# Optimization experiments

Measured on AMD Instinct MI355X. Metric: run time of the kernel, lower is better.

Reference implementation:

```python
import jax, jax.numpy as jnp
import numpy as np


def _hippo_dplr(n):
    # HiPPO-LegS -> NPLR -> DPLR (diagonal plus low rank) init, as in S4
    pr = np.sqrt(1.0 + 2.0 * np.arange(n))
    A = -(np.tril(pr[:, None] * pr[None, :]) - np.diag(np.arange(n)))
    p = np.sqrt(np.arange(n) + 0.5)
    b = np.sqrt(2.0 * np.arange(n) + 1.0)
    S = A + p[:, None] * p[None, :]
    lam_re = np.full(n, np.mean(np.diagonal(S)))
    lam_im, V = np.linalg.eigh(S * -1j)  # S*-1j is Hermitian
    p_c = V.conj().T @ p.astype(np.complex128)
    b_c = V.conj().T @ b.astype(np.complex128)
    return lam_re, lam_im, p_c, b_c


def setup_inputs():
    B, L, H, N = 4, 1024, 512, 64
    key = jax.random.key(0)
    kx, kc, ks, k1, k2 = jax.random.split(key, 5)
    lam_re, lam_im, p_c, b_c = _hippo_dplr(N)
    c = jax.random.normal(kc, (N, 2)) * (0.5 ** 0.5)
    f32 = lambda a: jnp.asarray(a, dtype=jnp.float32)
    return {
        'x': jax.random.normal(kx, (B, L, H), dtype=jnp.float32),
        'norm_weight': jnp.ones((H,), jnp.float32),
        'norm_bias': jnp.zeros((H,), jnp.float32),
        'lambda_re': f32(lam_re), 'lambda_im': f32(lam_im),
        'p_re': f32(p_c.real), 'p_im': f32(p_c.imag),
        'b_re': f32(b_c.real), 'b_im': f32(b_c.imag),
        'c_re': c[:, 0].astype(jnp.float32), 'c_im': c[:, 1].astype(jnp.float32),
        'd': jnp.ones((), jnp.float32),
        'log_step': jax.random.uniform(ks, (), jnp.float32, float(np.log(0.001)), float(np.log(0.1))),
        'out_w': (jax.random.normal(k1, (H, H), jnp.float32) / np.sqrt(H)).astype(jnp.float32),
        'out_b': jnp.zeros((H,), jnp.float32),
        'out2_w': (jax.random.normal(k2, (H, H), jnp.float32) / np.sqrt(H)).astype(jnp.float32),
        'out2_b': jnp.zeros((H,), jnp.float32),
    }


def reference(x, norm_weight, norm_bias, lambda_re, lambda_im, p_re, p_im,
              b_re, b_im, c_re, c_im, d, log_step, out_w, out_b, out2_w, out2_b):
    Bsz, L, H = x.shape
    skip = x
    # LayerNorm over channel dim (eps=1e-5, eqx default)
    mu = jnp.mean(x, -1, keepdims=True)
    var = jnp.mean((x - mu) ** 2, -1, keepdims=True)
    xn = (x - mu) / jnp.sqrt(var + 1e-5) * norm_weight + norm_bias
    # --- S4 DPLR bilinear discretization ---
    lam = (lambda_re + 1j * lambda_im).astype(jnp.complex64)
    p = (p_re + 1j * p_im).astype(jnp.complex64)
    b = (b_re + 1j * b_im).astype(jnp.complex64)
    c = (c_re + 1j * c_im).astype(jnp.complex64)
    step = jnp.exp(log_step).astype(jnp.complex64)
    N = lam.shape[0]
    I = jnp.eye(N, dtype=jnp.complex64)
    A = jnp.diag(lam) - p[:, None] * p[None, :].conj()
    A0 = (2.0 / step) * I + A
    Dinv = jnp.diag(1.0 / ((2.0 / step) - lam))
    qcD = p.conj()[None, :] @ Dinv           # [1,N]
    Dp = Dinv @ p[:, None]                   # [N,1]
    A1 = Dinv - (Dp @ qcD) / (1.0 + (qcD @ p[:, None]))  # Woodbury
    Ab = A1 @ A0                             # [N,N] discrete state matrix
    Bb = 2.0 * (A1 @ b[:, None])[:, 0]       # [N]
    # --- sequential state-space scan over time, vectorized over (B,H) lanes ---
    u = xn.astype(jnp.complex64)             # [B,L,H]

    def step_fn(state, u_t):                 # state: [B,H,N], u_t: [B,H]
        new = jnp.einsum('nm,bhm->bhn', Ab, state) + u_t[..., None] * Bb
        return new, jnp.einsum('n,bhn->bh', c, new).real

    init = jnp.zeros((Bsz, H, N), jnp.complex64)
    _, ys = jax.lax.scan(step_fn, init, jnp.moveaxis(u, 1, 0))  # ys: [L,B,H]
    y = jnp.moveaxis(ys, 0, 1) + d * xn      # feedthrough term
    # --- GELU + GLU-style gated output projection, residual ---
    y = jax.nn.gelu(y)
    gate = jax.nn.sigmoid(y @ out2_w.T + out2_b)
    return skip + (y @ out_w.T + out_b) * gate
```

## Files before the change

kernel.cpp:

```cpp
#include <hip/hip_runtime.h>
#include <hip/hip_bf16.h>
#include <math.h>

#define HDIM 512
#define LSEQ 1024
#define BSZ  4

typedef __attribute__((ext_vector_type(8))) short short8;
typedef __attribute__((ext_vector_type(4))) float floatx4;
typedef _Float16 half8 __attribute__((ext_vector_type(8)));

__device__ __forceinline__ float2 cmul(float2 a, float2 b) {
  float2 r;
  r.x = a.x * b.x - a.y * b.y;
  r.y = a.x * b.y + a.y * b.x;
  return r;
}
__device__ __forceinline__ float2 cadd(float2 a, float2 b) {
  float2 r; r.x = a.x + b.x; r.y = a.y + b.y; return r;
}
__device__ __forceinline__ float2 cfma(float2 a, float2 b, float2 c) {
  c.x += a.x * b.x - a.y * b.y;
  c.y += a.x * b.y + a.y * b.x;
  return c;
}
__device__ __forceinline__ ushort f2h(float f) {
  _Float16 h = (_Float16)f;
  return *(ushort*)&h;
}

__global__ __launch_bounds__(576) void stage1_kernel(
    const float* __restrict__ x, const float* __restrict__ nw,
    const float* __restrict__ nb, float* __restrict__ xn,
    const float* __restrict__ lre, const float* __restrict__ lim,
    const float* __restrict__ pre, const float* __restrict__ pim,
    const float* __restrict__ bre, const float* __restrict__ bim,
    const float* __restrict__ cre, const float* __restrict__ cim,
    const float* __restrict__ logstep, float* __restrict__ Kout,
    const float* __restrict__ w1, const float* __restrict__ w2,
    ushort* __restrict__ Wst) {
  __shared__ float2 Ldab[64], Lu[64], Lr[64], LBb[64];
  __shared__ float2 Rv[2048];
  __shared__ float2 Wv[2048];
  int tid = threadIdx.x;
  int wv = tid >> 6;
  int lane = tid & 63;

  if (blockIdx.x != 0) {
    int row = (blockIdx.x - 1) * 9 + wv;
    if (row < BSZ * LSEQ) {
      const float* xr = x + (size_t)row * HDIM;
      float4 v0 = ((const float4*)xr)[lane];
      float4 v1 = ((const float4*)xr)[lane + 64];
      float s  = v0.x + v0.y + v0.z + v0.w + v1.x + v1.y + v1.z + v1.w;
      float ss = v0.x*v0.x + v0.y*v0.y + v0.z*v0.z + v0.w*v0.w
               + v1.x*v1.x + v1.y*v1.y + v1.z*v1.z + v1.w*v1.w;
      #pragma unroll
      for (int m = 1; m < 64; m <<= 1) { s += __shfl_xor(s, m); ss += __shfl_xor(ss, m); }
      float mu   = s * (1.0f / HDIM);
      float var  = ss * (1.0f / HDIM) - mu * mu;
      float rstd = rsqrtf(var + 1e-5f);
      float4 w0 = ((const float4*)nw)[lane];
      float4 w1v = ((const float4*)nw)[lane + 64];
      float4 b0 = ((const float4*)nb)[lane];
      float4 b1 = ((const float4*)nb)[lane + 64];
      float4 o0, o1;
      o0.x = (v0.x - mu) * rstd * w0.x + b0.x;
      o0.y = (v0.y - mu) * rstd * w0.y + b0.y;
      o0.z = (v0.z - mu) * rstd * w0.z + b0.z;
      o0.w = (v0.w - mu) * rstd * w0.w + b0.w;
      o1.x = (v1.x - mu) * rstd * w1v.x + b1.x;
      o1.y = (v1.y - mu) * rstd * w1v.y + b1.y;
      o1.z = (v1.z - mu) * rstd * w1v.z + b1.z;
      o1.w = (v1.w - mu) * rstd * w1v.w + b1.w;
      float* xo = xn + (size_t)row * HDIM;
      ((float4*)xo)[lane] = o0;
      ((float4*)xo)[lane + 64] = o1;
    }
    int idx = (blockIdx.x - 1) * 576 + tid;
    if (idx < 65536) {
      int e0 = idx * 8;
      int n = e0 >> 9, k0 = e0 & 511;
      const float* Wr = (n < 512) ? (w1 + (size_t)n * 512 + k0)
                                  : (w2 + (size_t)(n - 512) * 512 + k0);
      ushort tmp[8];
      #pragma unroll
      for (int q = 0; q < 8; q++) tmp[q] = f2h(Wr[q]);
      *(short8*)&Wst[e0] = *(short8*)tmp;
    }
    return;
  }

  if (tid < 64) {
    int n = tid;
    float step = expf(logstep[0]);
    float g = 2.0f / step;
    float lr = lre[n], li = lim[n];
    float pr = pre[n], pi = pim[n];
    float br = bre[n], bi = bim[n];
    float den  = (g - lr) * (g - lr) + li * li;
    float dinr = (g - lr) / den, dini = li / den;
    float dabr = (g + lr) * dinr - li * dini;
    float dabi = (g + lr) * dini + li * dinr;
    float ur = dinr * pr - dini * pi;
    float ui = dinr * pi + dini * pr;
    float qr = pr * dinr + pi * dini;
    float qi = pr * dini - pi * dinr;
    float pm2 = pr * pr + pi * pi;
    float betr = pm2 * dinr, beti = pm2 * dini;
    float gar = qr * br - qi * bi;
    float gai = qr * bi + qi * br;
    #pragma unroll
    for (int m = 1; m < 64; m <<= 1) {
      betr += __shfl_xor(betr, m); beti += __shfl_xor(beti, m);
      gar  += __shfl_xor(gar, m);  gai  += __shfl_xor(gai, m);
    }
    float obr = 1.0f + betr, obi = beti;
    float ob2 = obr * obr + obi * obi;
    float kr = -2.0f * g * obr / ob2;
    float ki =  2.0f * g * obi / ob2;
    float rr = kr * qr - ki * qi;
    float ri = kr * qi + ki * qr;
    float tgr = (gar * obr + gai * obi) / ob2;
    float tgi = (gai * obr - gar * obi) / ob2;
    float dbr = dinr * br - dini * bi;
    float dbi = dinr * bi + dini * br;
    float Bbr = 2.0f * (dbr - (ur * tgr - ui * tgi));
    float Bbi = 2.0f * (dbi - (ur * tgi + ui * tgr));
    float2 t;
    t.x = dabr; t.y = dabi; Ldab[n] = t;
    t.x = ur;   t.y = ui;   Lu[n]   = t;
    t.x = rr;   t.y = ri;   Lr[n]   = t;
    t.x = Bbr;  t.y = Bbi;  LBb[n]  = t;
  }
  if (wv == 8) { float2 cc; cc.x = cre[lane]; cc.y = cim[lane]; Rv[lane] = cc; }
  __syncthreads();

  int g8 = lane >> 3;
  int q8 = lane & 7;
  int jm = wv * 8 + g8;
  float2 cv[8];

  if (wv < 8) {
    float2 dab[8], u[8], rn[8];
    #pragma unroll
    for (int ii = 0; ii < 8; ii++) {
      int n = q8 * 8 + ii;
      dab[ii] = Ldab[n]; u[ii] = Lu[n]; rn[ii] = Lr[n];
    }
    float2 rj = Lr[jm];
    #pragma unroll
    for (int ii = 0; ii < 8; ii++) {
      int n = q8 * 8 + ii;
      cv[ii] = cmul(u[ii], rj);
      if (n == jm) cv[ii] = cadd(cv[ii], dab[ii]);
    }
    for (int s = 0; s < 31; s++) {
      float2 part; part.x = 0.f; part.y = 0.f;
      #pragma unroll
      for (int ii = 0; ii < 8; ii++) part = cfma(rn[ii], cv[ii], part);
      #pragma unroll
      for (int m = 1; m < 8; m <<= 1) {
        part.x += __shfl_xor(part.x, m);
        part.y += __shfl_xor(part.y, m);
      }
      #pragma unroll
      for (int ii = 0; ii < 8; ii++) {
        float2 nc = cmul(dab[ii], cv[ii]);
        cv[ii] = cfma(u[ii], part, nc);
      }
    }
  } else {
    float2 dab0 = Ldab[lane], u0 = Lu[lane], r0 = Lr[lane];
    float2 w = LBb[lane];
    Wv[lane * 32 + 0] = w;
    for (int b = 1; b < 32; b++) {
      float dr = r0.x * w.x - r0.y * w.y;
      float di = r0.x * w.y + r0.y * w.x;
      #pragma unroll
      for (int m = 1; m < 64; m <<= 1) { dr += __shfl_xor(dr, m); di += __shfl_xor(di, m); }
      float2 nw2;
      nw2.x = dab0.x * w.x - dab0.y * w.y + u0.x * dr - u0.y * di;
      nw2.y = dab0.x * w.y + dab0.y * w.x + u0.x * di + u0.y * dr;
      w = nw2;
      Wv[lane * 32 + b] = w;
    }
  }
  __syncthreads();

  for (int a = 1; a < 32; a++) {
    if (wv < 8) {
      float2 part; part.x = 0.f; part.y = 0.f;
      #pragma unroll
      for (int ii = 0; ii < 8; ii++) {
        float2 Rk = Rv[(a - 1) * 64 + q8 * 8 + ii];
        part = cfma(Rk, cv[ii], part);
      }
      #pragma unroll
      for (int m = 1; m < 8; m <<= 1) {
        part.x += __shfl_xor(part.x, m);
        part.y += __shfl_xor(part.y, m);
      }
      if (q8 == 0) Rv[a * 64 + jm] = part;
    }
    __syncthreads();
  }

  for (int midx = tid; midx < 1024; midx += 576) {
    int a = midx >> 5, b = midx & 31;
    float acc = 0.f;
    for (int n = 0; n < 64; n++) {
      float2 R = Rv[a * 64 + n];
      float2 W = Wv[n * 32 + b];
      acc += R.x * W.x - R.y * W.y;
    }
    Kout[midx] = acc;
  }
}

__global__ __launch_bounds__(256) void prep_kernel(
    const float* __restrict__ xn, const float* __restrict__ K,
    ushort* __restrict__ Uhi, ushort* __restrict__ Thi) {
  __shared__ float tile[64][65];
  int blk = blockIdx.x;
  int tid = threadIdx.x;
  if (blk < 512) {
    int ht = blk & 7, lt = (blk >> 3) & 15, b = blk >> 7;
    #pragma unroll
    for (int q = 0; q < 16; q++) {
      int idx = q * 256 + tid;
      int r = idx >> 6, c = idx & 63;
      tile[r][c] = xn[((size_t)(b * LSEQ + lt * 64 + r)) * HDIM + ht * 64 + c];
    }
    __syncthreads();
    #pragma unroll
    for (int q = 0; q < 16; q++) {
      int idx = q * 256 + tid;
      int r = idx >> 6, c = idx & 63;
      size_t off = ((size_t)(b * HDIM + ht * 64 + r)) * LSEQ + lt * 64 + c;
      Uhi[off] = f2h(tile[c][r]);
    }
  } else {
    int r = blk - 512;
    int t = r * 2 + (tid >> 7);
    int tau0 = (tid & 127) * 8;
    ushort hi[8];
    #pragma unroll
    for (int q = 0; q < 8; q++) {
      int tau = tau0 + q;
      float v = (tau <= t) ? K[t - tau] : 0.f;
      hi[q] = f2h(v);
    }
    *(short8*)&Thi[(size_t)t * 1024 + tau0] = *(short8*)hi;
  }
}

__global__ __launch_bounds__(256) void conv_gemm_kernel(
    const ushort* __restrict__ Thi, const ushort* __restrict__ Uhi,
    const float* __restrict__ xn, const float* __restrict__ dptr,
    ushort* __restrict__ A) {
  __shared__ ushort sbuf[2 * 5120];
  int tid = threadIdx.x;
  int lane = tid & 63;
  int wv = tid >> 6;
  int wm = wv >> 1, wn = wv & 1;
  int by = blockIdx.y;
  int bm = (by < 8) ? by : 23 - by;
  int bn = blockIdx.x;
  floatx4 acc[2][2] = {};
  int srow = tid >> 2;
  int scol = (tid & 3) * 8;
  int ldst = srow * 40 + scol;
  int fr = lane & 15, fq = (lane >> 4) * 8;
  size_t Toff = (size_t)(bm * 64 + srow) * 1024 + scol;
  size_t Uoff = (size_t)(bn * 64 + srow) * 1024 + scol;
  int KT = 2 * (bm + 1);
  {
    uint4 th = *(const uint4*)&Thi[Toff];
    uint4 uh = *(const uint4*)&Uhi[Uoff];
    *(uint4*)&sbuf[ldst]        = th;
    *(uint4*)&sbuf[ldst + 2560] = uh;
  }
  __syncthreads();
  for (int kt = 0; kt < KT; kt++) {
    int cur = kt & 1;
    uint4 nth = {}, nuh = {};
    if (kt + 1 < KT) {
      size_t k1 = (size_t)(kt + 1) * 32;
      nth = *(const uint4*)&Thi[Toff + k1];
      nuh = *(const uint4*)&Uhi[Uoff + k1];
    }
    const ushort* sTh = sbuf + cur * 5120;
    const ushort* sUh = sTh + 2560;
    half8 ah[2], bh[2];
    #pragma unroll
    for (int i = 0; i < 2; i++) {
      ah[i] = *(const half8*)&sTh[(wm * 32 + i * 16 + fr) * 40 + fq];
      bh[i] = *(const half8*)&sUh[(wn * 32 + i * 16 + fr) * 40 + fq];
    }
    #pragma unroll
    for (int i = 0; i < 2; i++)
      #pragma unroll
      for (int j = 0; j < 2; j++)
        acc[i][j] = __builtin_amdgcn_mfma_f32_16x16x32_f16(ah[i], bh[j], acc[i][j], 0, 0, 0);
    if (kt + 1 < KT) {
      ushort* dst = sbuf + (cur ^ 1) * 5120;
      *(uint4*)&dst[ldst]        = nth;
      *(uint4*)&dst[ldst + 2560] = nuh;
      __syncthreads();
    }
  }
  float d = dptr[0];
  int row0 = bm * 64 + wm * 32;
  int col0 = bn * 64 + wn * 32;
  int fc = lane & 15, frq = (lane >> 4) * 4;
  #pragma unroll
  for (int i = 0; i < 2; i++)
    #pragma unroll
    for (int j = 0; j < 2; j++)
      #pragma unroll
      for (int r = 0; r < 4; r++) {
        int t = row0 + i * 16 + frq + r;
        int c = col0 + j * 16 + fc;
        int b = c >> 9, h = c & 511;
        size_t off = (size_t)(b * LSEQ + t) * HDIM + h;
        float y = acc[i][j][r] + d * xn[off];
        float tnh = tanhf(0.7978845608028654f * (y + 0.044715f * y * y * y));
        A[off] = f2h(0.5f * y * (1.0f + tnh));
      }
}

__global__ __launch_bounds__(256) void proj_kernel(
    const ushort* __restrict__ Abuf, const ushort* __restrict__ Wst,
    const float* __restrict__ x, const float* __restrict__ ob,
    const float* __restrict__ o2b, float* __restrict__ out) {
  __shared__ ushort sbuf[2 * 7680];
  int tid = threadIdx.x;
  int lane = tid & 63;
  int wv = tid >> 6;
  int wm = wv >> 1, wn = wv & 1;
  int bm = blockIdx.y, bn = blockIdx.x;
  int srow = tid >> 2;
  int scol = (tid & 3) * 8;
  int ldst = srow * 40 + scol;
  int fr = lane & 15, fq = (lane >> 4) * 8;
  floatx4 acc1[2][2] = {}, acc2[2][2] = {};
  size_t Aoff  = (size_t)(bm * 64 + srow) * 512 + scol;
  size_t W1off = (size_t)(bn * 64 + srow) * 512 + scol;
  size_t W2off = W1off + (size_t)512 * 512;
  {
    uint4 a0 = *(const uint4*)&Abuf[Aoff];
    uint4 v1 = *(const uint4*)&Wst[W1off];
    uint4 v2 = *(const uint4*)&Wst[W2off];
    *(uint4*)&sbuf[ldst]        = a0;
    *(uint4*)&sbuf[ldst + 2560] = v1;
    *(uint4*)&sbuf[ldst + 5120] = v2;
  }
  __syncthreads();
  for (int kt = 0; kt < 16; kt++) {
    int cur = kt & 1;
    uint4 na = {}, n1 = {}, n2 = {};
    if (kt + 1 < 16) {
      int k1 = (kt + 1) * 32;
      na = *(const uint4*)&Abuf[Aoff + k1];
      n1 = *(const uint4*)&Wst[W1off + k1];
      n2 = *(const uint4*)&Wst[W2off + k1];
    }
    const ushort* sA  = sbuf + cur * 7680;
    const ushort* sW1 = sA + 2560;
    const ushort* sW2 = sA + 5120;
    half8 af[2], b1[2], b2[2];
    #pragma unroll
    for (int i = 0; i < 2; i++) {
      af[i] = *(const half8*)&sA[(wm * 32 + i * 16 + fr) * 40 + fq];
      b1[i] = *(const half8*)&sW1[(wn * 32 + i * 16 + fr) * 40 + fq];
      b2[i] = *(const half8*)&sW2[(wn * 32 + i * 16 + fr) * 40 + fq];
    }
    #pragma unroll
    for (int i = 0; i < 2; i++)
      #pragma unroll
      for (int j = 0; j < 2; j++) {
        acc1[i][j] = __builtin_amdgcn_mfma_f32_16x16x32_f16(af[i], b1[j], acc1[i][j], 0, 0, 0);
        acc2[i][j] = __builtin_amdgcn_mfma_f32_16x16x32_f16(af[i], b2[j], acc2[i][j], 0, 0, 0);
      }
    if (kt + 1 < 16) {
      ushort* dst = sbuf + (cur ^ 1) * 7680;
      *(uint4*)&dst[ldst]        = na;
      *(uint4*)&dst[ldst + 2560] = n1;
      *(uint4*)&dst[ldst + 5120] = n2;
      __syncthreads();
    }
  }
  int row0 = bm * 64 + wm * 32;
  int col0 = bn * 64 + wn * 32;
  int fc = lane & 15, frq = (lane >> 4) * 4;
  #pragma unroll
  for (int i = 0; i < 2; i++)
    #pragma unroll
    for (int j = 0; j < 2; j++)
      #pragma unroll
      for (int r = 0; r < 4; r++) {
        int row = row0 + i * 16 + frq + r;
        int col = col0 + j * 16 + fc;
        float c1 = acc1[i][j][r] + ob[col];
        float c2 = acc2[i][j][r] + o2b[col];
        float gate = 1.0f / (1.0f + expf(-c2));
        size_t off = (size_t)row * HDIM + col;
        out[off] = x[off] + c1 * gate;
      }
}

extern "C" void kernel_launch(void* const* d_in, const int* in_sizes, int n_in,
                              void* d_out, int out_size, void* d_ws, size_t ws_size,
                              hipStream_t stream) {
  const float* x   = (const float*)d_in[0];
  const float* nw  = (const float*)d_in[1];
  const float* nb  = (const float*)d_in[2];
  const float* lre = (const float*)d_in[3];
  const float* lim = (const float*)d_in[4];
  const float* pre = (const float*)d_in[5];
  const float* pim = (const float*)d_in[6];
  const float* bre = (const float*)d_in[7];
  const float* bim = (const float*)d_in[8];
  const float* cre = (const float*)d_in[9];
  const float* cim = (const float*)d_in[10];
  const float* dsc = (const float*)d_in[11];
  const float* lst = (const float*)d_in[12];
  const float* w1  = (const float*)d_in[13];
  const float* ob  = (const float*)d_in[14];
  const float* w2  = (const float*)d_in[15];
  const float* o2b = (const float*)d_in[16];

  char* ws = (char*)d_ws;
  float* xn    = (float*)(ws);
  ushort* Uhi  = (ushort*)(ws + (size_t)(8  << 20));
  ushort* Thi  = (ushort*)(ws + (size_t)(12 << 20));
  ushort* Wst  = (ushort*)(ws + (size_t)(16 << 20));
  ushort* Abuf = (ushort*)(ws + (size_t)(17 << 20));
  float* Kbuf  = (float*)(ws + (size_t)(21 << 20));
  float* out   = (float*)d_out;

  stage1_kernel<<<dim3(457), dim3(576), 0, stream>>>(x, nw, nb, xn,
                                                     lre, lim, pre, pim, bre, bim,
                                                     cre, cim, lst, Kbuf,
                                                     w1, w2, Wst);
  prep_kernel<<<dim3(1024), dim3(256), 0, stream>>>(xn, Kbuf, Uhi, Thi);
  conv_gemm_kernel<<<dim3(32, 16), dim3(256), 0, stream>>>(Thi, Uhi,
                                                           xn, dsc, Abuf);
  proj_kernel<<<dim3(8, 64), dim3(256), 0, stream>>>(Abuf, Wst, x, ob, o2b, out);
}
```

Baseline: 160.0 us.

## Fuse prep kernel into conv GEMM: build Toeplitz and transposed U tiles on the fly

Removes the separate prep kernel that materialized the fp16 Toeplitz matrix and a transposed fp16 copy of the normalized input. The conv GEMM now builds Toeplitz tiles directly from the kernel vector K (zero-padded at the front so negative indices read zeros) and gathers the normalized input transposed into LDS from an fp16 buffer. The LayerNorm output is stored in fp16 instead of fp32, halving its traffic, but the d*xn feedthrough now uses the fp16 value, which reduces accuracy. The per-element scalar gathers in the GEMM loop may be less efficient than the previous vector loads.

After: 170.5 us. 1.07x slower.

```diff
diff --git a/kernel.cpp b/kernel.cpp
--- a/kernel.cpp
+++ b/kernel.cpp
@@ -1,5 +1,4 @@
 #include <hip/hip_runtime.h>
-#include <hip/hip_bf16.h>
 #include <math.h>
 
 #define HDIM 512
@@ -28,15 +27,18 @@
   _Float16 h = (_Float16)f;
   return *(ushort*)&h;
 }
+__device__ __forceinline__ uint pack2h(float a, float b) {
+  return (uint)f2h(a) | ((uint)f2h(b) << 16);
+}
 
 __global__ __launch_bounds__(576) void stage1_kernel(
     const float* __restrict__ x, const float* __restrict__ nw,
-    const float* __restrict__ nb, float* __restrict__ xn,
+    const float* __restrict__ nb, ushort* __restrict__ xn16,
     const float* __restrict__ lre, const float* __restrict__ lim,
     const float* __restrict__ pre, const float* __restrict__ pim,
     const float* __restrict__ bre, const float* __restrict__ bim,
     const float* __restrict__ cre, const float* __restrict__ cim,
-    const float* __restrict__ logstep, float* __restrict__ Kout,
+    const float* __restrict__ logstep, float* __restrict__ Kbuf,
     const float* __restrict__ w1, const float* __restrict__ w2,
     ushort* __restrict__ Wst) {
   __shared__ float2 Ldab[64], Lu[64], Lr[64], LBb[64];
@@ -73,9 +75,12 @@
       o1.y = (v1.y - mu) * rstd * w1v.y + b1.y;
       o1.z = (v1.z - mu) * rstd * w1v.z + b1.z;
       o1.w = (v1.w - mu) * rstd * w1v.w + b1.w;
-      float* xo = xn + (size_t)row * HDIM;
-      ((float4*)xo)[lane] = o0;
-      ((float4*)xo)[lane + 64] = o1;
+      ushort* xo = xn16 + (size_t)row * HDIM;
+      uint2 p0, p1;
+      p0.x = pack2h(o0.x, o0.y); p0.y = pack2h(o0.z, o0.w);
+      p1.x = pack2h(o1.x, o1.y); p1.y = pack2h(o1.z, o1.w);
+      *(uint2*)&xo[lane * 4]       = p0;
+      *(uint2*)&xo[256 + lane * 4] = p1;
     }
     int idx = (blockIdx.x - 1) * 576 + tid;
     if (idx < 65536) {
@@ -134,6 +139,7 @@
     t.x = Bbr;  t.y = Bbi;  LBb[n]  = t;
   }
   if (wv == 8) { float2 cc; cc.x = cre[lane]; cc.y = cim[lane]; Rv[lane] = cc; }
+  if (tid < 64) Kbuf[tid] = 0.f;
   __syncthreads();
 
   int g8 = lane >> 3;
@@ -214,52 +220,15 @@
       float2 W = Wv[n * 32 + b];
       acc += R.x * W.x - R.y * W.y;
     }
-    Kout[midx] = acc;
-  }
-}
-
-__global__ __launch_bounds__(256) void prep_kernel(
-    const float* __restrict__ xn, const float* __restrict__ K,
-    ushort* __restrict__ Uhi, ushort* __restrict__ Thi) {
-  __shared__ float tile[64][65];
-  int blk = blockIdx.x;
-  int tid = threadIdx.x;
-  if (blk < 512) {
-    int ht = blk & 7, lt = (blk >> 3) & 15, b = blk >> 7;
-    #pragma unroll
-    for (int q = 0; q < 16; q++) {
-      int idx = q * 256 + tid;
-      int r = idx >> 6, c = idx & 63;
-      tile[r][c] = xn[((size_t)(b * LSEQ + lt * 64 + r)) * HDIM + ht * 64 + c];
-    }
-    __syncthreads();
-    #pragma unroll
-    for (int q = 0; q < 16; q++) {
-      int idx = q * 256 + tid;
-      int r = idx >> 6, c = idx & 63;
-      size_t off = ((size_t)(b * HDIM + ht * 64 + r)) * LSEQ + lt * 64 + c;
-      Uhi[off] = f2h(tile[c][r]);
-    }
-  } else {
-    int r = blk - 512;
-    int t = r * 2 + (tid >> 7);
-    int tau0 = (tid & 127) * 8;
-    ushort hi[8];
-    #pragma unroll
-    for (int q = 0; q < 8; q++) {
-      int tau = tau0 + q;
-      float v = (tau <= t) ? K[t - tau] : 0.f;
-      hi[q] = f2h(v);
-    }
-    *(short8*)&Thi[(size_t)t * 1024 + tau0] = *(short8*)hi;
+    Kbuf[64 + midx] = acc;
   }
 }
 
 __global__ __launch_bounds__(256) void conv_gemm_kernel(
-    const ushort* __restrict__ Thi, const ushort* __restrict__ Uhi,
-    const float* __restrict__ xn, const float* __restrict__ dptr,
-    ushort* __restrict__ A) {
-  __shared__ ushort sbuf[2 * 5120];
+    const ushort* __restrict__ xn16, const float* __restrict__ Kbuf,
+    const float* __restrict__ dptr, ushort* __restrict__ A) {
+  __shared__ __attribute__((aligned(16))) ushort sbuf[2 * 5120];
+  const float* Kp = Kbuf + 64;
   int tid = threadIdx.x;
   int lane = tid & 63;
   int wv = tid >> 6;
@@ -267,28 +236,51 @@
   int by = blockIdx.y;
   int bm = (by < 8) ? by : 23 - by;
   int bn = blockIdx.x;
+  int b  = bn >> 3;
+  int h0 = (bn & 7) * 64;
   floatx4 acc[2][2] = {};
   int srow = tid >> 2;
   int scol = (tid & 3) * 8;
-  int ldst = srow * 40 + scol;
+  int trow = bm * 64 + srow;
+  int rr = lane & 3;
+  int ng = lane >> 2;
+  int k0 = (wv * 4 + rr) * 2;
   int fr = lane & 15, fq = (lane >> 4) * 8;
-  size_t Toff = (size_t)(bm * 64 + srow) * 1024 + scol;
-  size_t Uoff = (size_t)(bn * 64 + srow) * 1024 + scol;
   int KT = 2 * (bm + 1);
+
   {
-    uint4 th = *(const uint4*)&Thi[Toff];
-    uint4 uh = *(const uint4*)&Uhi[Uoff];
-    *(uint4*)&sbuf[ldst]        = th;
-    *(uint4*)&sbuf[ldst + 2560] = uh;
+    int base = trow - scol;
+    float kv[8];
+    #pragma unroll
+    for (int q = 0; q < 8; q++) kv[q] = Kp[base - q];
+    uint4 tw;
+    tw.x = pack2h(kv[0], kv[1]); tw.y = pack2h(kv[2], kv[3]);
+    tw.z = pack2h(kv[4], kv[5]); tw.w = pack2h(kv[6], kv[7]);
+    *(uint4*)&sbuf[srow * 40 + scol] = tw;
+    const ushort* ra = xn16 + ((size_t)(b * LSEQ + k0) * HDIM) + h0;
+    const ushort* rb = ra + HDIM;
+    #pragma unroll
+    for (int j = 0; j < 4; j++) {
+      int n = ng + 16 * j;
+      uint wj = (uint)ra[n] | ((uint)rb[n] << 16);
+      *(uint*)&sbuf[2560 + n * 40 + k0] = wj;
+    }
   }
   __syncthreads();
   for (int kt = 0; kt < KT; kt++) {
     int cur = kt & 1;
-    uint4 nth = {}, nuh = {};
+    float kv[8]; uint bw[4];
     if (kt + 1 < KT) {
-      size_t k1 = (size_t)(kt + 1) * 32;
-      nth = *(const uint4*)&Thi[Toff + k1];
-      nuh = *(const uint4*)&Uhi[Uoff + k1];
+      int base = trow - (kt + 1) * 32 - scol;
+      #pragma unroll
+      for (int q = 0; q < 8; q++) kv[q] = Kp[base - q];
+      const ushort* ra = xn16 + ((size_t)(b * LSEQ + (kt + 1) * 32 + k0) * HDIM) + h0;
+      const ushort* rb = ra + HDIM;
+      #pragma unroll
+      for (int j = 0; j < 4; j++) {
+        int n = ng + 16 * j;
+        bw[j] = (uint)ra[n] | ((uint)rb[n] << 16);
+      }
     }
     const ushort* sTh = sbuf + cur * 5120;
     const ushort* sUh = sTh + 2560;
@@ -305,8 +297,15 @@
         acc[i][j] = __builtin_amdgcn_mfma_f32_16x16x32_f16(ah[i], bh[j], acc[i][j], 0, 0, 0);
     if (kt + 1 < KT) {
       ushort* dst = sbuf + (cur ^ 1) * 5120;
-      *(uint4*)&dst[ldst]        = nth;
-      *(uint4*)&dst[ldst + 2560] = nuh;
+      uint4 tw;
+      tw.x = pack2h(kv[0], kv[1]); tw.y = pack2h(kv[2], kv[3]);
+      tw.z = pack2h(kv[4], kv[5]); tw.w = pack2h(kv[6], kv[7]);
+      *(uint4*)&dst[srow * 40 + scol] = tw;
+      #pragma unroll
+      for (int j = 0; j < 4; j++) {
+        int n = ng + 16 * j;
+        *(uint*)&dst[2560 + n * 40 + k0] = bw[j];
+      }
       __syncthreads();
     }
   }
@@ -322,9 +321,10 @@
       for (int r = 0; r < 4; r++) {
         int t = row0 + i * 16 + frq + r;
         int c = col0 + j * 16 + fc;
-        int b = c >> 9, h = c & 511;
-        size_t off = (size_t)(b * LSEQ + t) * HDIM + h;
-        float y = acc[i][j][r] + d * xn[off];
+        int bb = c >> 9, h = c & 511;
+        size_t off = (size_t)(bb * LSEQ + t) * HDIM + h;
+        float xv = (float)(*(const _Float16*)&xn16[off]);
+        float y = acc[i][j][r] + d * xv;
         float tnh = tanhf(0.7978845608028654f * (y + 0.044715f * y * y * y));
         A[off] = f2h(0.5f * y * (1.0f + tnh));
       }
@@ -334,7 +334,7 @@
     const ushort* __restrict__ Abuf, const ushort* __restrict__ Wst,
     const float* __restrict__ x, const float* __restrict__ ob,
     const float* __restrict__ o2b, float* __restrict__ out) {
-  __shared__ ushort sbuf[2 * 7680];
+  __shared__ __attribute__((aligned(16))) ushort sbuf[2 * 7680];
   int tid = threadIdx.x;
   int lane = tid & 63;
   int wv = tid >> 6;
@@ -432,20 +432,16 @@
   const float* o2b = (const float*)d_in[16];
 
   char* ws = (char*)d_ws;
-  float* xn    = (float*)(ws);
-  ushort* Uhi  = (ushort*)(ws + (size_t)(8  << 20));
-  ushort* Thi  = (ushort*)(ws + (size_t)(12 << 20));
+  ushort* xn16 = (ushort*)(ws);
+  float* Kbuf  = (float*)(ws + (size_t)(8 << 20));
   ushort* Wst  = (ushort*)(ws + (size_t)(16 << 20));
   ushort* Abuf = (ushort*)(ws + (size_t)(17 << 20));
-  float* Kbuf  = (float*)(ws + (size_t)(21 << 20));
   float* out   = (float*)d_out;
 
-  stage1_kernel<<<dim3(457), dim3(576), 0, stream>>>(x, nw, nb, xn,
+  stage1_kernel<<<dim3(457), dim3(576), 0, stream>>>(x, nw, nb, xn16,
                                                      lre, lim, pre, pim, bre, bim,
                                                      cre, cim, lst, Kbuf,
                                                      w1, w2, Wst);
-  prep_kernel<<<dim3(1024), dim3(256), 0, stream>>>(xn, Kbuf, Uhi, Thi);
-  conv_gemm_kernel<<<dim3(32, 16), dim3(256), 0, stream>>>(Thi, Uhi,
-                                                           xn, dsc, Abuf);
+  conv_gemm_kernel<<<dim3(32, 16), dim3(256), 0, stream>>>(xn16, Kbuf, dsc, Abuf);
   proj_kernel<<<dim3(8, 64), dim3(256), 0, stream>>>(Abuf, Wst, x, ob, o2b, out);
 }
```
